# Kernel tuning notes

Measured on AMD Instinct MI355X. Metric: run time of the kernel, lower is better.

Reference implementation:

```python
import jax, jax.numpy as jnp
import numpy as np

INPUT_SIZE = 512
HIDDEN = 1024
N_QP = 64
M_QP = 128
QP_ITER = 50
MIN_EIG = 0.01
N_P = N_QP * (N_QP + 1) // 2              # 2080
N_H = M_QP * N_QP                          # 8192
N_OUT = N_P + N_QP + N_H + M_QP            # 10464
BATCH = 1024


def setup_inputs() -> dict:
    key = jax.random.key(0)
    ks = jax.random.split(key, 4)
    s = lambda fan_in: np.float32(1.0 / np.sqrt(fan_in))
    return {
        "x": jax.random.normal(ks[0], (BATCH, INPUT_SIZE), jnp.float32),
        "W1": jax.random.normal(ks[1], (INPUT_SIZE, HIDDEN), jnp.float32) * s(INPUT_SIZE),
        "b1": jnp.zeros((HIDDEN,), jnp.float32),
        "W2": jax.random.normal(ks[2], (HIDDEN, HIDDEN), jnp.float32) * s(HIDDEN),
        "b2": jnp.zeros((HIDDEN,), jnp.float32),
        "W3": jax.random.normal(ks[3], (HIDDEN, N_OUT), jnp.float32) * s(HIDDEN),
        "b3": jnp.zeros((N_OUT,), jnp.float32),
    }


def _make_psd(p):
    # p: (bs, n(n+1)/2) packed row-major lower triangle of Cholesky factor L.
    # Diagonal entries (index i(i+1)/2 - 1) -> sqrt(min_eig) + softplus, so P = L L' is PSD.
    bs = p.shape[0]
    i = jnp.arange(1, N_QP + 1)
    diag_idx = i * (i + 1) // 2 - 1
    p = p.at[:, diag_idx].set(np.float32(np.sqrt(MIN_EIG)) + jax.nn.softplus(p[:, diag_idx]))
    r, c = jnp.tril_indices(N_QP)
    L = jnp.zeros((bs, N_QP, N_QP), p.dtype).at[:, r, c].set(p)
    return jnp.einsum('bik,bjk->bij', L, L)


def _forward(x, W1, b1, W2, b2, W3, b3):
    # MLP generating QP parameters (P, q, H, b)
    h = jax.nn.relu(x @ W1 + b1)
    h = jax.nn.relu(h @ W2 + b2)
    out = h @ W3 + b3                               # (bs, N_OUT)
    P_params = out[:, :N_P]
    q = out[:, N_P:N_P + N_QP]                      # (bs, n)
    H = out[:, N_P + N_QP:N_P + N_QP + N_H].reshape(-1, M_QP, N_QP)  # (bs, m, n)
    b = out[:, N_P + N_QP + N_H:]                   # (bs, m)
    P = _make_psd(P_params)                         # (bs, n, n)

    # Step sizes: tau = sigma = 0.9 / ||H||_2, spectral norm via 10 fixed power iterations
    v = jnp.ones((x.shape[0], N_QP), x.dtype) / np.float32(np.sqrt(N_QP))
    for _ in range(10):
        w = jnp.einsum('bmn,bm->bn', H, jnp.einsum('bmn,bn->bm', H, v))
        v = w / (jnp.linalg.norm(w, axis=1, keepdims=True) + 1e-12)
    sn = jnp.linalg.norm(jnp.einsum('bmn,bn->bm', H, v), axis=1) + 1e-6
    tau = (0.9 / sn)[:, None]                       # (bs, 1) primal step
    sig = tau                                       # dual step

    # Precompute (I + tau P)^{-1} once; fixed across PDHG iterations
    eye = jnp.eye(N_QP, dtype=x.dtype)
    Minv = jnp.linalg.inv(eye[None] + tau[:, :, None] * P)

    x0 = jnp.zeros((x.shape[0], N_QP), x.dtype)
    lam0 = jnp.zeros((x.shape[0], M_QP), x.dtype)

    def step(carry, _):
        xp, xbar, lam = carry
        lam = jax.nn.relu(lam - sig * (jnp.einsum('bmn,bn->bm', H, xbar) + b))
        xn = jnp.einsum('bnk,bk->bn', Minv, xp + tau * (jnp.einsum('bmn,bm->bn', H, lam) - q))
        return (xn, 2.0 * xn - xp, lam), None

    (xs, _, _), _ = jax.lax.scan(step, (x0, x0, lam0), None, length=QP_ITER)
    return xs  # (bs, n_qp): last primal iterate, matching solver(...)[1][:, -1, :]


def reference(x, W1, b1, W2, b2, W3, b3):
    return _forward(x, W1, b1, W2, b2, W3, b3)
```

## Files before the change

kernel.cpp:

```cpp
#include <hip/hip_runtime.h>
#include <cstdint>

typedef unsigned short u16;
typedef __attribute__((ext_vector_type(8))) short short8;
typedef __attribute__((ext_vector_type(4))) float floatx4;
typedef __attribute__((ext_vector_type(4))) float f4;

#define NQP   64
#define MQP   128
#define NP    2080
#define NHH   8192
#define NOUT  10464
#define NOUTP 10496

__device__ __forceinline__ float b2f(u16 u) {
  union { unsigned int i; float f; } v; v.i = ((unsigned int)u) << 16; return v.f;
}
__device__ __forceinline__ u16 f2b(float f) {
  union { float f; unsigned int i; } v; v.f = f;
  unsigned int r = v.i + 0x7fffu + ((v.i >> 16) & 1u);
  return (u16)(r >> 16);
}

__global__ __launch_bounds__(256) void detect_dtype(const u16* __restrict__ w,
                                                    int* __restrict__ flag) {
  __shared__ int cnt;
  if (threadIdx.x == 0) cnt = 0;
  __syncthreads();
  int c = 0;
  for (int i = threadIdx.x; i < 16384; i += 256) {
    const int e = (w[i] >> 7) & 0xFF;
    if (e >= 130 || e <= 90) ++c;
  }
  atomicAdd(&cnt, c);
  __syncthreads();
  if (threadIdx.x == 0) flag[0] = (cnt > 3000) ? 1 : 0;
}

__device__ __forceinline__ u16 load_elem_bf16(const void* p, size_t idx, int isf32) {
  return isf32 ? f2b(((const float*)p)[idx]) : ((const u16*)p)[idx];
}

__global__ __launch_bounds__(256) void convert_bf16(const void* __restrict__ in,
                                                    u16* __restrict__ out, int n,
                                                    const int* __restrict__ flag) {
  const int isf = flag[0];
  for (int i = blockIdx.x * 256 + threadIdx.x; i < n; i += gridDim.x * 256)
    out[i] = load_elem_bf16(in, i, isf);
}

__global__ __launch_bounds__(256) void convert_f32(const void* __restrict__ in,
                                                   float* __restrict__ out, int n,
                                                   const int* __restrict__ flag) {
  const int isf = flag[0];
  for (int i = blockIdx.x * 256 + threadIdx.x; i < n; i += gridDim.x * 256)
    out[i] = isf ? ((const float*)in)[i] : b2f(((const u16*)in)[i]);
}

__global__ __launch_bounds__(256) void transpose_pad(const void* __restrict__ in,
                                                     u16* __restrict__ out,
                                                     int K, int N, int Npad,
                                                     const int* __restrict__ flag) {
  __shared__ u16 tile[32][33];
  const int isf = flag[0];
  const int n0 = blockIdx.x * 32, k0 = blockIdx.y * 32;
  const int tx = threadIdx.x & 31, ty = threadIdx.x >> 5;
#pragma unroll
  for (int i = 0; i < 4; ++i) {
    const int k = k0 + ty + 8 * i, n = n0 + tx;
    tile[ty + 8 * i][tx] = (n < N) ? load_elem_bf16(in, (size_t)k * N + n, isf) : (u16)0;
  }
  __syncthreads();
#pragma unroll
  for (int i = 0; i < 4; ++i) {
    const int n = n0 + ty + 8 * i, k = k0 + tx;
    if (n < Npad) out[(size_t)n * K + k] = tile[tx][ty + 8 * i];
  }
}

__device__ __forceinline__ void gload_lds16(const u16* g, u16* l) {
  __builtin_amdgcn_global_load_lds((const __attribute__((address_space(1))) void*)g,
                                   (__attribute__((address_space(3))) void*)l, 16, 0, 0);
}

template <int EPI, bool HAS_LO>
__global__ __launch_bounds__(256) void gemm_bt(const u16* __restrict__ Ahi, const u16* __restrict__ Alo,
                                               const u16* __restrict__ Bt,  const float* __restrict__ bias,
                                               u16* __restrict__ Chi, u16* __restrict__ Clo,
                                               float* __restrict__ Cf,
                                               int M, int N, int K) {
  __shared__ __align__(16) u16 lA[128 * 32];
  __shared__ __align__(16) u16 lAlo[128 * 32];
  __shared__ __align__(16) u16 lB[128 * 32];
  const int tile_n = blockIdx.x * 128;
  const int tile_m = blockIdx.y * 128;
  const int lane = threadIdx.x & 63;
  const int wv   = threadIdx.x >> 6;
  const int wm = (wv & 1) * 64;
  const int wn = (wv >> 1) * 64;
  const int sr = lane >> 2;
  const int sk = (lane & 3) * 8;
  floatx4 acc[4][4] = {};

  for (int k0 = 0; k0 < K; k0 += 32) {
#pragma unroll
    for (int it = 0; it < 2; ++it) {
      const int slot = it * 4 + wv;
      const int r = slot * 16 + sr;
      gload_lds16(Ahi + (size_t)(tile_m + r) * K + k0 + sk, lA + slot * 512);
      if (HAS_LO)
        gload_lds16(Alo + (size_t)(tile_m + r) * K + k0 + sk, lAlo + slot * 512);
      gload_lds16(Bt + (size_t)(tile_n + r) * K + k0 + sk, lB + slot * 512);
    }
    __syncthreads();
    const int ro = lane & 15;
    const int qo = (lane >> 4) * 8;
    short8 af[4], bfr[4], al[4];
#pragma unroll
    for (int i = 0; i < 4; ++i) af[i] = *(const short8*)(lA + (wm + i * 16 + ro) * 32 + qo);
#pragma unroll
    for (int j = 0; j < 4; ++j) bfr[j] = *(const short8*)(lB + (wn + j * 16 + ro) * 32 + qo);
    if (HAS_LO) {
#pragma unroll
      for (int i = 0; i < 4; ++i) al[i] = *(const short8*)(lAlo + (wm + i * 16 + ro) * 32 + qo);
    }
#pragma unroll
    for (int i = 0; i < 4; ++i)
#pragma unroll
      for (int j = 0; j < 4; ++j) {
        acc[i][j] = __builtin_amdgcn_mfma_f32_16x16x32_bf16(af[i], bfr[j], acc[i][j], 0, 0, 0);
        if (HAS_LO)
          acc[i][j] = __builtin_amdgcn_mfma_f32_16x16x32_bf16(al[i], bfr[j], acc[i][j], 0, 0, 0);
      }
    __syncthreads();
  }

  const int colb = tile_n + wn + (lane & 15);
  const int rowb = tile_m + wm + (lane >> 4) * 4;
#pragma unroll
  for (int j = 0; j < 4; ++j) {
    const int col = colb + j * 16;
    const float bv = (col < N) ? bias[col] : 0.f;
#pragma unroll
    for (int i = 0; i < 4; ++i) {
#pragma unroll
      for (int v = 0; v < 4; ++v) {
        const int row = rowb + i * 16 + v;
        float val = acc[i][j][v] + bv;
        if (EPI == 0) {
          val = fmaxf(val, 0.f);
          const u16 hi = f2b(val);
          const float lo = val - b2f(hi);
          Chi[(size_t)row * N + col] = hi;
          Clo[(size_t)row * N + col] = f2b(lo);
        } else {
          if (col < N) Cf[(size_t)row * N + col] = val;
        }
      }
    }
  }
}

__device__ __forceinline__ f4 ld4s(const float* p) { return *(const f4*)p; }
__device__ __forceinline__ void st4s(float* p, f4 v) { *(f4*)p = v; }
__device__ __forceinline__ float dot4(f4 a, f4 b) {
  return fmaf(a.x, b.x, fmaf(a.y, b.y, fmaf(a.z, b.z, a.w * b.w)));
}
__device__ __forceinline__ f4 shx4(f4 v, int m) {
  f4 r;
  r.x = __shfl_xor(v.x, m, 64); r.y = __shfl_xor(v.y, m, 64);
  r.z = __shfl_xor(v.z, m, 64); r.w = __shfl_xor(v.w, m, 64);
  return r;
}
__device__ __forceinline__ int hQ(int m, int g) {
  return (m << 6) + (((g ^ (m & 15))) << 2);
}

__global__ __launch_bounds__(256, 4) void qp_solve(const float* __restrict__ outbuf,
                                                   void* __restrict__ xs,
                                                   const int* __restrict__ flag) {
  __shared__ __align__(16) float H_s[8192];
  __shared__ __align__(16) float lam_s[128];
  __shared__ __align__(16) float b_s[128];
  __shared__ __align__(16) float part_s[4][64];
  __shared__ __align__(16) float xb2[2][64];
  __shared__ __align__(16) float xp2[2][64];
  __shared__ __align__(16) float q_s[64];
  __shared__ __align__(16) float buf2[2][64];
  __shared__ float tau_sh;

  const int t = threadIdx.x;
  const int w = t >> 6, l = t & 63;
  const int am = 32 * w + (l >> 1), as = l & 1;
  const int bg = l & 15, bc = l >> 4;
  const int ci = 16 * w + (l >> 2), cc = l & 3;
  const int isf = flag[0];
  const float* ob = outbuf + (size_t)blockIdx.x * NOUT;

  float* Ld = H_s;
  float* ps = H_s + 4352;
  for (int e = t; e < 4352; e += 256) Ld[e] = 0.f;
  for (int e = t; e < NP; e += 256) ps[e] = ob[e];
  if (t < 64) q_s[t] = ob[NP + t];
  if (t >= 128 && t < 256) b_s[t - 128] = ob[NP + NQP + NHH + (t - 128)];
  __syncthreads();
  if (t < 64) {
    const int i = t + 1;
    const int d = i * (i + 1) / 2 - 1;
    const float xv = ps[d];
    ps[d] = 0.1f + (fmaxf(xv, 0.f) + log1pf(expf(-fabsf(xv))));
  }
  __syncthreads();
  for (int e = t; e < NP; e += 256) {
    int i = (int)((sqrtf(8.f * (float)e + 1.f) - 1.f) * 0.5f);
    while ((i + 1) * (i + 2) / 2 <= e) ++i;
    while (i * (i + 1) / 2 > e) --i;
    const int j = e - i * (i + 1) / 2;
    Ld[i * 68 + j] = ps[e];
  }
  __syncthreads();

  float M[16];
#pragma unroll
  for (int jj = 0; jj < 16; ++jj) M[jj] = 0.f;
#pragma unroll
  for (int h = 0; h < 2; ++h) {
    f4 Lr[8];
#pragma unroll
    for (int g = 0; g < 8; ++g) Lr[g] = ld4s(&Ld[ci * 68 + (h * 8 + g) * 4]);
#pragma unroll
    for (int jj = 0; jj < 16; ++jj) {
      const int j = 16 * cc + jj;
      float s = 0.f;
#pragma unroll
      for (int g = 0; g < 8; ++g) s += dot4(Lr[g], ld4s(&Ld[j * 68 + (h * 8 + g) * 4]));
      M[jj] += s;
    }
  }
  __syncthreads();

  for (int e = t; e < NHH; e += 256) {
    const int m = e >> 6, n = e & 63;
    H_s[hQ(m, n >> 2) + (n & 3)] = ob[NP + NQP + e];
  }
  if (t < 64) { xb2[0][t] = 0.125f; }
  __syncthreads();

  for (int pi = 0; pi < 10; ++pi) {
    {
      float s = 0.f;
#pragma unroll
      for (int k = 0; k < 8; ++k) {
        const int g = 8 * as + k;
        s += dot4(ld4s(&H_s[hQ(am, g)]), ld4s(&xb2[0][4 * g]));
      }
      s += __shfl_xor(s, 1, 64);
      if (as == 0) lam_s[am] = s;
    }
    __syncthreads();
    {
      f4 u = {0.f, 0.f, 0.f, 0.f};
#pragma unroll
      for (int k = 0; k < 8; ++k) {
        const int m = 32 * w + 8 * bc + k;
        u += ld4s(&H_s[hQ(m, bg)]) * lam_s[m];
      }
      u += shx4(u, 16); u += shx4(u, 32);
      if (l < 16) st4s(&part_s[w][4 * bg], u);
    }
    __syncthreads();
    if (t < 64) {
      const float u = part_s[0][t] + part_s[1][t] + part_s[2][t] + part_s[3][t];
      float ss = u * u;
#pragma unroll
      for (int o = 1; o <= 32; o <<= 1) ss += __shfl_xor(ss, o, 64);
      xb2[0][t] = u / (sqrtf(ss) + 1e-12f);
    }
    __syncthreads();
  }
  {
    float s = 0.f;
#pragma unroll
    for (int k = 0; k < 8; ++k) {
      const int g = 8 * as + k;
      s += dot4(ld4s(&H_s[hQ(am, g)]), ld4s(&xb2[0][4 * g]));
    }
    s += __shfl_xor(s, 1, 64);
    if (as == 0) lam_s[am] = s;
  }
  __syncthreads();
  if (t < 64) {
    const float a = lam_s[t], bb = lam_s[t + 64];
    float ss = a * a + bb * bb;
#pragma unroll
    for (int o = 1; o <= 32; o <<= 1) ss += __shfl_xor(ss, o, 64);
    if (t == 0) tau_sh = 0.9f / (sqrtf(ss) + 1e-6f);
  }
  __syncthreads();
  const float tau = tau_sh;

#pragma unroll
  for (int jj = 0; jj < 16; ++jj)
    M[jj] = tau * M[jj] + ((16 * cc + jj == ci) ? 1.0f : 0.0f);

  if (ci == 0) {
#pragma unroll
    for (int jj = 0; jj < 16; ++jj) buf2[0][16 * cc + jj] = M[jj];
  }
  __syncthreads();
#pragma unroll
  for (int k = 0; k < 64; ++k) {
    const int kb = k & 1;
    const int kc = k >> 4;
    const float d = 1.0f / buf2[kb][k];
    f4 rv[4];
#pragma unroll
    for (int u = 0; u < 4; ++u) rv[u] = ld4s(&buf2[kb][16 * cc + 4 * u]);
    const float f = __shfl(M[k & 15], (l & 60) | kc, 64);
    if (ci == k) {
#pragma unroll
      for (int jj = 0; jj < 16; ++jj) M[jj] = rv[jj >> 2][jj & 3] * d;
      if (cc == kc) M[k & 15] = d;
    } else {
#pragma unroll
      for (int jj = 0; jj < 16; ++jj)
        M[jj] = fmaf(-f, rv[jj >> 2][jj & 3] * d, M[jj]);
      if (cc == kc) M[k & 15] = -f * d;
    }
    if (k < 63 && ci == k + 1) {
#pragma unroll
      for (int jj = 0; jj < 16; ++jj) buf2[1 - kb][16 * cc + jj] = M[jj];
    }
    __syncthreads();
  }

  float c0;
  {
    float acc = 0.f;
#pragma unroll
    for (int u = 0; u < 4; ++u) {
      const f4 qv = ld4s(&q_s[16 * cc + 4 * u]);
      acc = fmaf(M[4 * u + 0], qv.x, acc);
      acc = fmaf(M[4 * u + 1], qv.y, acc);
      acc = fmaf(M[4 * u + 2], qv.z, acc);
      acc = fmaf(M[4 * u + 3], qv.w, acc);
    }
    acc += __shfl_xor(acc, 1, 64);
    acc += __shfl_xor(acc, 2, 64);
    c0 = tau * acc;
  }

  if (t < 64) { xb2[0][t] = 0.f; xp2[0][t] = 0.f; }
  float lam = 0.f, xpr = 0.f;
  const float br = b_s[am];
  __syncthreads();

  for (int it = 0; it < 50; ++it) {
    const int p = it & 1;
    {
      float s = 0.f;
#pragma unroll
      for (int k = 0; k < 8; ++k) {
        const int g = 8 * as + k;
        s += dot4(ld4s(&H_s[hQ(am, g)]), ld4s(&xb2[p][4 * g]));
      }
      s += __shfl_xor(s, 1, 64);
      lam = fmaxf(lam - tau * (s + br), 0.f);
      if (as == 0) lam_s[am] = lam;
    }
    __syncthreads();
    {
      f4 u = {0.f, 0.f, 0.f, 0.f};
#pragma unroll
      for (int k = 0; k < 8; ++k) {
        const int m = 32 * w + 8 * bc + k;
        u += ld4s(&H_s[hQ(m, bg)]) * lam_s[m];
      }
      u += shx4(u, 16); u += shx4(u, 32);
      if (l < 16) st4s(&part_s[w][4 * bg], u);
    }
    __syncthreads();
    {
      float acc = 0.f;
#pragma unroll
      for (int u = 0; u < 4; ++u) {
        const int j4 = 16 * cc + 4 * u;
        const f4 uv = ld4s(&part_s[0][j4]) + ld4s(&part_s[1][j4]) +
                      ld4s(&part_s[2][j4]) + ld4s(&part_s[3][j4]);
        const f4 rv = ld4s(&xp2[p][j4]) + uv * tau;
        acc = fmaf(M[4 * u + 0], rv.x, acc);
        acc = fmaf(M[4 * u + 1], rv.y, acc);
        acc = fmaf(M[4 * u + 2], rv.z, acc);
        acc = fmaf(M[4 * u + 3], rv.w, acc);
      }
      acc += __shfl_xor(acc, 1, 64);
      acc += __shfl_xor(acc, 2, 64);
      if (cc == 0) {
        const float xn = acc - c0;
        xp2[1 - p][ci] = xn;
        xb2[1 - p][ci] = 2.f * xn - xpr;
        xpr = xn;
      }
    }
    __syncthreads();
  }

  if (cc == 0) {
    const size_t oi = (size_t)blockIdx.x * NQP + ci;
    if (isf) ((float*)xs)[oi] = xpr;
    else     ((u16*)xs)[oi]   = f2b(xpr);
  }
}

extern "C" void kernel_launch(void* const* d_in, const int* in_sizes, int n_in,
                              void* d_out, int out_size, void* d_ws, size_t ws_size,
                              hipStream_t stream) {
  const void* x  = d_in[0];
  const void* W1 = d_in[1];
  const void* b1 = d_in[2];
  const void* W2 = d_in[3];
  const void* b2 = d_in[4];
  const void* W3 = d_in[5];
  const void* b3 = d_in[6];

  char* ws = (char*)d_ws;
  size_t off = 0;
  auto take = [&](size_t bytes) -> char* {
    char* r = ws + off;
    off += (bytes + 255) & ~(size_t)255;
    return r;
  };
  int*   flag = (int*)take(256);
  float* bf1  = (float*)take(1024 * 4);
  float* bf2  = (float*)take(1024 * 4);
  float* bf3  = (float*)take((size_t)NOUT * 4);
  u16*   W3t  = (u16*)take((size_t)NOUTP * 1024 * 2);
  u16*   h2hi = (u16*)take(1024ull * 1024 * 2);
  u16*   h2lo = (u16*)take(1024ull * 1024 * 2);
  char*  region = take(1024ull * NOUT * 4);
  float* outf = (float*)region;
  u16* xb   = (u16*)(region + 0);
  u16* W1t  = (u16*)(region + (1u << 20));
  u16* W2t  = (u16*)(region + (2u << 20));
  u16* h1hi = (u16*)(region + (4u << 20));
  u16* h1lo = (u16*)(region + (6u << 20));
  (void)ws_size; (void)in_sizes; (void)n_in; (void)out_size;

  detect_dtype<<<dim3(1), 256, 0, stream>>>((const u16*)W1, flag);

  convert_bf16<<<dim3(512), 256, 0, stream>>>(x, xb, 1024 * 512, flag);
  convert_f32<<<dim3(4), 256, 0, stream>>>(b1, bf1, 1024, flag);
  convert_f32<<<dim3(4), 256, 0, stream>>>(b2, bf2, 1024, flag);
  convert_f32<<<dim3(41), 256, 0, stream>>>(b3, bf3, NOUT, flag);

  transpose_pad<<<dim3(32, 16), 256, 0, stream>>>(W1, W1t, 512, 1024, 1024, flag);
  transpose_pad<<<dim3(32, 32), 256, 0, stream>>>(W2, W2t, 1024, 1024, 1024, flag);
  transpose_pad<<<dim3(NOUTP / 32, 32), 256, 0, stream>>>(W3, W3t, 1024, NOUT, NOUTP, flag);

  gemm_bt<0, false><<<dim3(8, 8), 256, 0, stream>>>(xb, nullptr, W1t, bf1,
                                                    h1hi, h1lo, nullptr, 1024, 1024, 512);
  gemm_bt<0, true><<<dim3(8, 8), 256, 0, stream>>>(h1hi, h1lo, W2t, bf2,
                                                   h2hi, h2lo, nullptr, 1024, 1024, 1024);
  gemm_bt<1, true><<<dim3(NOUTP / 128, 8), 256, 0, stream>>>(h2hi, h2lo, W3t, bf3,
                                                             nullptr, nullptr, outf, 1024, NOUT, 1024);
  qp_solve<<<dim3(1024), 256, 0, stream>>>(outf, d_out, flag);
}
```

Before: 519.2 us.

## Merge bias/transpose prep launches and compute PDHG rhs once per iteration

Fuses the three bias conversion kernels into one launch and the three weight transposes into one combined-grid launch, cutting launch count and the serialization between small kernels. In the QP solver, the per-iteration rhs (xp + tau*H^T lam) is now built once by 64 threads into shared memory, instead of every thread reducing the four partial sums itself. The double-buffered x arrays become single buffers. This adds an extra __syncthreads per iteration, and writing xp_s/xb_s in place depends on the barrier ordering to stay correct.

```diff
diff --git a/kernel.cpp b/kernel.cpp
--- a/kernel.cpp
+++ b/kernel.cpp
@@ -49,21 +49,42 @@
     out[i] = load_elem_bf16(in, i, isf);
 }
 
-__global__ __launch_bounds__(256) void convert_f32(const void* __restrict__ in,
-                                                   float* __restrict__ out, int n,
+__global__ __launch_bounds__(256) void conv_biases(const void* __restrict__ b1,
+                                                   const void* __restrict__ b2,
+                                                   const void* __restrict__ b3,
+                                                   float* __restrict__ bf1,
+                                                   float* __restrict__ bf2,
+                                                   float* __restrict__ bf3,
                                                    const int* __restrict__ flag) {
   const int isf = flag[0];
-  for (int i = blockIdx.x * 256 + threadIdx.x; i < n; i += gridDim.x * 256)
-    out[i] = isf ? ((const float*)in)[i] : b2f(((const u16*)in)[i]);
-}
-
-__global__ __launch_bounds__(256) void transpose_pad(const void* __restrict__ in,
-                                                     u16* __restrict__ out,
-                                                     int K, int N, int Npad,
+  const int i = blockIdx.x * 256 + threadIdx.x;
+  if (i < 1024) {
+    bf1[i] = isf ? ((const float*)b1)[i] : b2f(((const u16*)b1)[i]);
+  } else if (i < 2048) {
+    const int j = i - 1024;
+    bf2[j] = isf ? ((const float*)b2)[j] : b2f(((const u16*)b2)[j]);
+  } else if (i < 2048 + NOUT) {
+    const int j = i - 2048;
+    bf3[j] = isf ? ((const float*)b3)[j] : b2f(((const u16*)b3)[j]);
+  }
+}
+
+__global__ __launch_bounds__(256) void transpose_all(const void* __restrict__ W1,
+                                                     const void* __restrict__ W2,
+                                                     const void* __restrict__ W3,
+                                                     u16* __restrict__ W1t,
+                                                     u16* __restrict__ W2t,
+                                                     u16* __restrict__ W3t,
                                                      const int* __restrict__ flag) {
+  const int bx = blockIdx.x, by = blockIdx.y;
+  const void* in; u16* out; int K, N, Npad, bxo;
+  if (bx < 32)      { in = W1; out = W1t; K = 512;  N = 1024; Npad = 1024;  bxo = 0;
+                      if (by >= 16) return; }
+  else if (bx < 64) { in = W2; out = W2t; K = 1024; N = 1024; Npad = 1024;  bxo = 32; }
+  else              { in = W3; out = W3t; K = 1024; N = NOUT; Npad = NOUTP; bxo = 64; }
   __shared__ u16 tile[32][33];
   const int isf = flag[0];
-  const int n0 = blockIdx.x * 32, k0 = blockIdx.y * 32;
+  const int n0 = (bx - bxo) * 32, k0 = by * 32;
   const int tx = threadIdx.x & 31, ty = threadIdx.x >> 5;
 #pragma unroll
   for (int i = 0; i < 4; ++i) {
@@ -183,8 +204,9 @@
   __shared__ __align__(16) float lam_s[128];
   __shared__ __align__(16) float b_s[128];
   __shared__ __align__(16) float part_s[4][64];
-  __shared__ __align__(16) float xb2[2][64];
-  __shared__ __align__(16) float xp2[2][64];
+  __shared__ __align__(16) float rhs_s[64];
+  __shared__ __align__(16) float xb_s[64];
+  __shared__ __align__(16) float xp_s[64];
   __shared__ __align__(16) float q_s[64];
   __shared__ __align__(16) float buf2[2][64];
   __shared__ float tau_sh;
@@ -243,7 +265,7 @@
     const int m = e >> 6, n = e & 63;
     H_s[hQ(m, n >> 2) + (n & 3)] = ob[NP + NQP + e];
   }
-  if (t < 64) { xb2[0][t] = 0.125f; }
+  if (t < 64) xb_s[t] = 0.125f;
   __syncthreads();
 
   for (int pi = 0; pi < 10; ++pi) {
@@ -252,7 +274,7 @@
 #pragma unroll
       for (int k = 0; k < 8; ++k) {
         const int g = 8 * as + k;
-        s += dot4(ld4s(&H_s[hQ(am, g)]), ld4s(&xb2[0][4 * g]));
+        s += dot4(ld4s(&H_s[hQ(am, g)]), ld4s(&xb_s[4 * g]));
       }
       s += __shfl_xor(s, 1, 64);
       if (as == 0) lam_s[am] = s;
@@ -274,7 +296,7 @@
       float ss = u * u;
 #pragma unroll
       for (int o = 1; o <= 32; o <<= 1) ss += __shfl_xor(ss, o, 64);
-      xb2[0][t] = u / (sqrtf(ss) + 1e-12f);
+      xb_s[t] = u / (sqrtf(ss) + 1e-12f);
     }
     __syncthreads();
   }
@@ -283,7 +305,7 @@
 #pragma unroll
     for (int k = 0; k < 8; ++k) {
       const int g = 8 * as + k;
-      s += dot4(ld4s(&H_s[hQ(am, g)]), ld4s(&xb2[0][4 * g]));
+      s += dot4(ld4s(&H_s[hQ(am, g)]), ld4s(&xb_s[4 * g]));
     }
     s += __shfl_xor(s, 1, 64);
     if (as == 0) lam_s[am] = s;
@@ -350,19 +372,18 @@
     c0 = tau * acc;
   }
 
-  if (t < 64) { xb2[0][t] = 0.f; xp2[0][t] = 0.f; }
+  if (t < 64) { xb_s[t] = 0.f; xp_s[t] = 0.f; }
   float lam = 0.f, xpr = 0.f;
   const float br = b_s[am];
   __syncthreads();
 
   for (int it = 0; it < 50; ++it) {
-    const int p = it & 1;
     {
       float s = 0.f;
 #pragma unroll
       for (int k = 0; k < 8; ++k) {
         const int g = 8 * as + k;
-        s += dot4(ld4s(&H_s[hQ(am, g)]), ld4s(&xb2[p][4 * g]));
+        s += dot4(ld4s(&H_s[hQ(am, g)]), ld4s(&xb_s[4 * g]));
       }
       s += __shfl_xor(s, 1, 64);
       lam = fmaxf(lam - tau * (s + br), 0.f);
@@ -380,14 +401,16 @@
       if (l < 16) st4s(&part_s[w][4 * bg], u);
     }
     __syncthreads();
+    if (t < 64) {
+      const float uu = part_s[0][t] + part_s[1][t] + part_s[2][t] + part_s[3][t];
+      rhs_s[t] = xp_s[t] + tau * uu;
+    }
+    __syncthreads();
     {
       float acc = 0.f;
 #pragma unroll
       for (int u = 0; u < 4; ++u) {
-        const int j4 = 16 * cc + 4 * u;
-        const f4 uv = ld4s(&part_s[0][j4]) + ld4s(&part_s[1][j4]) +
-                      ld4s(&part_s[2][j4]) + ld4s(&part_s[3][j4]);
-        const f4 rv = ld4s(&xp2[p][j4]) + uv * tau;
+        const f4 rv = ld4s(&rhs_s[16 * cc + 4 * u]);
         acc = fmaf(M[4 * u + 0], rv.x, acc);
         acc = fmaf(M[4 * u + 1], rv.y, acc);
         acc = fmaf(M[4 * u + 2], rv.z, acc);
@@ -397,8 +420,8 @@
       acc += __shfl_xor(acc, 2, 64);
       if (cc == 0) {
         const float xn = acc - c0;
-        xp2[1 - p][ci] = xn;
-        xb2[1 - p][ci] = 2.f * xn - xpr;
+        xp_s[ci] = xn;
+        xb_s[ci] = 2.f * xn - xpr;
         xpr = xn;
       }
     }
@@ -449,13 +472,8 @@
   detect_dtype<<<dim3(1), 256, 0, stream>>>((const u16*)W1, flag);
 
   convert_bf16<<<dim3(512), 256, 0, stream>>>(x, xb, 1024 * 512, flag);
-  convert_f32<<<dim3(4), 256, 0, stream>>>(b1, bf1, 1024, flag);
-  convert_f32<<<dim3(4), 256, 0, stream>>>(b2, bf2, 1024, flag);
-  convert_f32<<<dim3(41), 256, 0, stream>>>(b3, bf3, NOUT, flag);
-
-  transpose_pad<<<dim3(32, 16), 256, 0, stream>>>(W1, W1t, 512, 1024, 1024, flag);
-  transpose_pad<<<dim3(32, 32), 256, 0, stream>>>(W2, W2t, 1024, 1024, 1024, flag);
-  transpose_pad<<<dim3(NOUTP / 32, 32), 256, 0, stream>>>(W3, W3t, 1024, NOUT, NOUTP, flag);
+  conv_biases<<<dim3(49), 256, 0, stream>>>(b1, b2, b3, bf1, bf2, bf3, flag);
+  transpose_all<<<dim3(392, 32), 256, 0, stream>>>(W1, W2, W3, W1t, W2t, W3t, flag);
 
   gemm_bt<0, false><<<dim3(8, 8), 256, 0, stream>>>(xb, nullptr, W1t, bf1,
                                                     h1hi, h1lo, nullptr, 1024, 1024, 512);
```

Result: faster. 505.5 us (-2.6%).
